# Optimization experiments

Hardware: AMD Instinct MI355X
Metric: run time of the kernel (lower is better)

The kernel has to match this reference:

```python
import jax, jax.numpy as jnp
import numpy as np

N_SPK, N_UTT, D = 512, 64, 1024
EPS = 1e-6  # matches tf.math.l2_normalize default epsilon guard


def _l2norm(x, axis=-1):
    return x / jnp.sqrt(jnp.maximum(jnp.sum(x * x, axis=axis, keepdims=True), EPS))


def setup_inputs() -> dict:
    key = jax.random.key(0)
    k1, _ = jax.random.split(key)
    inputs = jax.random.normal(k1, (N_SPK, N_UTT, D), dtype=jnp.float32)
    w = jnp.asarray(10.0, dtype=jnp.float32)
    b = jnp.asarray(-5.0, dtype=jnp.float32)
    return {"inputs": inputs, "w": w, "b": b}


def reference(inputs, w, b):
    N, M, _ = inputs.shape
    # speaker centroids: mean over utterances -> [N, D]
    centroids = jnp.mean(inputs, axis=1)
    # utterance (exclusion) centroids: mean of the other M-1 utterances -> [N, M, D]
    ut_centroids = (jnp.sum(inputs, axis=1, keepdims=True) - inputs) / (M - 1)

    e = _l2norm(inputs)          # [N, M, D]
    c = _l2norm(centroids)       # [N, D]
    uc = _l2norm(ut_centroids)   # [N, M, D]

    # cosine sim of every utterance vs every speaker centroid -> [N, M, K]
    cos_all = jnp.einsum('nmd,kd->nmk', e, c)
    # same-speaker entries use the self-exclusion centroid
    cos_self = jnp.sum(e * uc, axis=-1)  # [N, M]
    eye = jnp.eye(N, dtype=inputs.dtype)[:, None, :]  # [N, 1, N]
    cos_sim = cos_all * (1.0 - eye) + cos_self[:, :, None] * eye

    sim = w * cos_sim + b  # [N, M, N]
    # softmax contrastive loss: -S_{j,i,j} + logsumexp_k S_{j,i,k}, summed
    lse = jax.nn.logsumexp(sim, axis=-1)            # [N, M]
    pos = jnp.einsum('nmn->nm', sim)                # diagonal along speaker axes
    loss = jnp.sum(lse - pos)
    return loss
```

## Files before the change

kernel.cpp:

```cpp
#include <hip/hip_runtime.h>
#include <stdint.h>

#define N_SPK 512
#define N_UTT 64
#define DIM   1024
#define NROWS (N_SPK * N_UTT)
#define EPS   1e-6f

#define BM  128
#define BN  128
#define BKB 128
#define KITERS (DIM / BKB)

typedef __attribute__((ext_vector_type(8))) int   int8v;
typedef __attribute__((ext_vector_type(4))) int   int4v;
typedef __attribute__((ext_vector_type(4))) float f32x4;

__global__ __launch_bounds__(256) void prep_full(
    const float* __restrict__ x, uint8_t* __restrict__ xb,
    uint8_t* __restrict__ cmat, float* __restrict__ xxg, float* __restrict__ ssqg)
{
    const int n    = blockIdx.x;
    const int tid  = threadIdx.x;
    const int lane = tid & 63;
    const int w    = tid >> 6;

    const float* xn  = x  + (size_t)n * N_UTT * DIM;
    uint8_t*     xbn = xb + (size_t)n * N_UTT * DIM;

    float Sp[16];
    #pragma unroll
    for (int j = 0; j < 16; ++j) Sp[j] = 0.f;

    for (int rnd = 0; rnd < 4; ++rnd) {
        const int m0 = w * 16 + rnd * 4;

        float4 v[16];
        #pragma unroll
        for (int i = 0; i < 4; ++i)
            #pragma unroll
            for (int j = 0; j < 4; ++j)
                v[i * 4 + j] = *(const float4*)(xn + (size_t)(m0 + i) * DIM + j * 256 + lane * 4);

        float xx[4] = {0.f, 0.f, 0.f, 0.f};
        #pragma unroll
        for (int i = 0; i < 4; ++i) {
            #pragma unroll
            for (int j = 0; j < 4; ++j) {
                const float4 q = v[i * 4 + j];
                xx[i] += q.x * q.x + q.y * q.y + q.z * q.z + q.w * q.w;
                Sp[j * 4 + 0] += q.x; Sp[j * 4 + 1] += q.y;
                Sp[j * 4 + 2] += q.z; Sp[j * 4 + 3] += q.w;
                uint32_t u = (uint32_t)__builtin_amdgcn_cvt_pk_fp8_f32(q.x, q.y, 0, false);
                u = (uint32_t)__builtin_amdgcn_cvt_pk_fp8_f32(q.z, q.w, (int)u, true);
                *(uint32_t*)(xbn + (size_t)(m0 + i) * DIM + j * 256 + lane * 4) = u;
            }
        }

        #pragma unroll
        for (int i = 0; i < 4; ++i) {
            float t = xx[i];
            #pragma unroll
            for (int off = 1; off < 64; off <<= 1) t += __shfl_xor(t, off);
            if (lane == 0) xxg[n * N_UTT + m0 + i] = t;
        }
    }

    __shared__ float Sh[4][DIM];
    #pragma unroll
    for (int j = 0; j < 4; ++j)
        *(float4*)&Sh[w][j * 256 + lane * 4] =
            make_float4(Sp[j * 4], Sp[j * 4 + 1], Sp[j * 4 + 2], Sp[j * 4 + 3]);
    __syncthreads();

    const int d0 = tid * 4;
    float4 S = *(const float4*)&Sh[0][d0];
    {
        const float4 b1 = *(const float4*)&Sh[1][d0];
        const float4 b2 = *(const float4*)&Sh[2][d0];
        const float4 b3 = *(const float4*)&Sh[3][d0];
        S.x += b1.x + b2.x + b3.x; S.y += b1.y + b2.y + b3.y;
        S.z += b1.z + b2.z + b3.z; S.w += b1.w + b2.w + b3.w;
    }

    float css = S.x * S.x + S.y * S.y + S.z * S.z + S.w * S.w;
    #pragma unroll
    for (int off = 1; off < 64; off <<= 1) css += __shfl_xor(css, off);
    __shared__ float red[4];
    if ((tid & 63) == 0) red[tid >> 6] = css;
    __syncthreads();
    const float ssq = red[0] + red[1] + red[2] + red[3];

    const float scale = rsqrtf(fmaxf(ssq * (1.0f / 4096.f), EPS)) * (16.0f / 64.f);
    uint32_t u = (uint32_t)__builtin_amdgcn_cvt_pk_fp8_f32(S.x * scale, S.y * scale, 0, false);
    u = (uint32_t)__builtin_amdgcn_cvt_pk_fp8_f32(S.z * scale, S.w * scale, (int)u, true);
    *(uint32_t*)(cmat + (size_t)n * DIM + d0) = u;
    if (tid == 0) ssqg[n] = ssq;
}

__global__ __launch_bounds__(256) void gemm_lse_kernel(
    const uint8_t* __restrict__ xb, const uint8_t* __restrict__ cmat,
    const float* __restrict__ xxg, const float* __restrict__ ssqg,
    const float* __restrict__ wp, const float* __restrict__ bp,
    float* __restrict__ sumexp4, float* __restrict__ pos)
{
    __shared__ __align__(16) uint8_t Asm[BM * BKB];
    __shared__ __align__(16) uint8_t Bsm[BN * BKB];
    __shared__ float SeLDS[BM];

    const int tid   = threadIdx.x;
    const int lane  = tid & 63;
    const int wid   = tid >> 6;
    const int waveM = wid >> 1;
    const int waveN = wid & 1;

    const int bid = blockIdx.x;
    const int rt  = (bid & 7) | ((bid >> 5) << 3);
    const int ct  = (bid >> 3) & 3;

    const int rowBase = rt * BM;
    const int colBase = ct * BN;

    const uint8_t* gA[4];
    const uint8_t* gB[4];
    #pragma unroll
    for (int i = 0; i < 4; ++i) {
        const int s    = i * 256 + tid;
        const int srow = s >> 3;
        const int h    = (s & 7) ^ (srow & 7);
        gA[i] = xb   + (size_t)(rowBase + srow) * DIM + h * 16;
        gB[i] = cmat + (size_t)(colBase + srow) * DIM + h * 16;
    }

    f32x4 acc[4][4];
    #pragma unroll
    for (int i = 0; i < 4; ++i)
        #pragma unroll
        for (int j = 0; j < 4; ++j)
            acc[i][j] = (f32x4){0.f, 0.f, 0.f, 0.f};

    const int cL  = lane & 15;
    const int q   = lane >> 4;
    const int fs0 = (2 * q) ^ (cL & 7);
    const int fs1 = fs0 ^ 1;

    for (int kt = 0; kt < KITERS; ++kt) {
        __syncthreads();
        const int ko = kt * BKB;
        #pragma unroll
        for (int i = 0; i < 4; ++i) {
            __builtin_amdgcn_global_load_lds(
                (const __attribute__((address_space(1))) void*)(gA[i] + ko),
                (__attribute__((address_space(3))) void*)(&Asm[(i * 256 + wid * 64) * 16]),
                16, 0, 0);
            __builtin_amdgcn_global_load_lds(
                (const __attribute__((address_space(1))) void*)(gB[i] + ko),
                (__attribute__((address_space(3))) void*)(&Bsm[(i * 256 + wid * 64) * 16]),
                16, 0, 0);
        }
        __syncthreads();

        int8v b[4];
        #pragma unroll
        for (int bj = 0; bj < 4; ++bj) {
            const int row = waveN * 64 + bj * 16 + cL;
            const int4v lo = *(const int4v*)&Bsm[row * BKB + fs0 * 16];
            const int4v hi = *(const int4v*)&Bsm[row * BKB + fs1 * 16];
            b[bj] = __builtin_shufflevector(lo, hi, 0, 1, 2, 3, 4, 5, 6, 7);
        }

        #pragma unroll
        for (int bi = 0; bi < 4; ++bi) {
            const int row = waveM * 64 + bi * 16 + cL;
            const int4v lo = *(const int4v*)&Asm[row * BKB + fs0 * 16];
            const int4v hi = *(const int4v*)&Asm[row * BKB + fs1 * 16];
            const int8v a = __builtin_shufflevector(lo, hi, 0, 1, 2, 3, 4, 5, 6, 7);
            #pragma unroll
            for (int bj = 0; bj < 4; ++bj)
                acc[bi][bj] = __builtin_amdgcn_mfma_scale_f32_16x16x128_f8f6f4(
                    a, b[bj], acc[bi][bj],
                    0, 0,
                    0, 0x7f7f7f7f,
                    0, 0x7f7f7f7f);
        }
    }

    const float wv = wp[0] * 0.0625f;
    const float bv = bp[0];
    float srow[16];
    #pragma unroll
    for (int bi = 0; bi < 4; ++bi) {
        #pragma unroll
        for (int r = 0; r < 4; ++r) {
            const int R     = rowBase + waveM * 64 + bi * 16 + q * 4 + r;
            const float xxv = xxg[R];
            const float rn  = rsqrtf(fmaxf(xxv, EPS));
            const int nrow  = R >> 6;
            float s = 0.f;
            #pragma unroll
            for (int bj = 0; bj < 4; ++bj) {
                const int col = colBase + waveN * 64 + bj * 16 + cL;
                const float dot = acc[bi][bj][r];
                float sim;
                if (col == nrow) {
                    const float ssqv = ssqg[nrow];
                    const float xs   = dot * sqrtf(ssqv) * 0.0625f;
                    const float d2   = ssqv - 2.f * xs + xxv;
                    const float cs   = ((xs - xxv) * (1.f / 63.f)) * rn *
                                       rsqrtf(fmaxf(d2 * (1.f / 3969.f), EPS));
                    sim = wp[0] * cs + bv;
                    pos[R] = sim;
                } else {
                    sim = wv * dot * rn + bv;
                }
                s += __expf(sim);
            }
            #pragma unroll
            for (int off = 1; off < 16; off <<= 1) s += __shfl_xor(s, off);
            srow[bi * 4 + r] = s;
        }
    }

    if (waveN == 1 && cL == 0) {
        #pragma unroll
        for (int bi = 0; bi < 4; ++bi)
            #pragma unroll
            for (int r = 0; r < 4; ++r)
                SeLDS[waveM * 64 + bi * 16 + q * 4 + r] = srow[bi * 4 + r];
    }
    __syncthreads();
    if (waveN == 0 && cL == 0) {
        #pragma unroll
        for (int bi = 0; bi < 4; ++bi)
            #pragma unroll
            for (int r = 0; r < 4; ++r) {
                const int lr = waveM * 64 + bi * 16 + q * 4 + r;
                sumexp4[(size_t)ct * NROWS + rowBase + lr] = srow[bi * 4 + r] + SeLDS[lr];
            }
    }
}

__global__ __launch_bounds__(1024) void finalize_kernel(
    const float* __restrict__ pos, const float* __restrict__ se4,
    float* __restrict__ out)
{
    const int tid = threadIdx.x;
    float acc = 0.f;
    for (int r = tid; r < NROWS; r += 1024) {
        const float s = se4[r] + se4[NROWS + r] + se4[2 * NROWS + r] + se4[3 * NROWS + r];
        acc += __logf(s) - pos[r];
    }
    #pragma unroll
    for (int off = 1; off < 64; off <<= 1) acc += __shfl_xor(acc, off);
    __shared__ float red[16];
    if ((tid & 63) == 0) red[tid >> 6] = acc;
    __syncthreads();
    if (tid == 0) {
        float t = 0.f;
        #pragma unroll
        for (int i = 0; i < 16; ++i) t += red[i];
        out[0] = t;
    }
}

extern "C" void kernel_launch(void* const* d_in, const int* in_sizes, int n_in,
                              void* d_out, int out_size, void* d_ws, size_t ws_size,
                              hipStream_t stream)
{
    const float* x  = (const float*)d_in[0];
    const float* wp = (const float*)d_in[1];
    const float* bp = (const float*)d_in[2];
    float* out = (float*)d_out;

    char* ws = (char*)d_ws;
    size_t off = 0;
    uint8_t*  xb      = (uint8_t*)(ws + off); off += (size_t)NROWS * DIM;
    uint8_t*  cmat    = (uint8_t*)(ws + off); off += (size_t)N_SPK * DIM;
    float*    xxg     = (float*)(ws + off);   off += (size_t)NROWS * 4;
    float*    pos     = (float*)(ws + off);   off += (size_t)NROWS * 4;
    float*    sumexp4 = (float*)(ws + off);   off += (size_t)4 * NROWS * 4;
    float*    ssqg    = (float*)(ws + off);   off += (size_t)N_SPK * 4;

    prep_full<<<N_SPK, 256, 0, stream>>>(x, xb, cmat, xxg, ssqg);
    gemm_lse_kernel<<<(NROWS / BM) * (N_SPK / BN), 256, 0, stream>>>(
        xb, cmat, xxg, ssqg, wp, bp, sumexp4, pos);
    finalize_kernel<<<1, 1024, 0, stream>>>(pos, sumexp4, out);
}
```

Measured before the change: 278.8 us.

## Process two column tiles per GEMM block, deepen prep loads, parallelize finalize

The GEMM grid is halved so each block loops over two consecutive column tiles. The A tile is reloaded for each tile, so this only changes scheduling and block count, with fewer blocks over the 256 CUs. The prep kernel now issues eight rows of loads per round instead of four, giving more memory-level parallelism at higher register cost. The finalize reduction is spread over 64 blocks that atomically add into an output zeroed by the prep kernel, which removes the serial single-block tail but makes the float summation order nondeterministic.

```diff
diff --git a/kernel.cpp b/kernel.cpp
--- a/kernel.cpp
+++ b/kernel.cpp
@@ -18,13 +18,16 @@
 
 __global__ __launch_bounds__(256) void prep_full(
     const float* __restrict__ x, uint8_t* __restrict__ xb,
-    uint8_t* __restrict__ cmat, float* __restrict__ xxg, float* __restrict__ ssqg)
+    uint8_t* __restrict__ cmat, float* __restrict__ xxg, float* __restrict__ ssqg,
+    float* __restrict__ out)
 {
     const int n    = blockIdx.x;
     const int tid  = threadIdx.x;
     const int lane = tid & 63;
     const int w    = tid >> 6;
 
+    if (n == 0 && tid == 0) out[0] = 0.f;
+
     const float* xn  = x  + (size_t)n * N_UTT * DIM;
     uint8_t*     xbn = xb + (size_t)n * N_UTT * DIM;
 
@@ -32,19 +35,22 @@
     #pragma unroll
     for (int j = 0; j < 16; ++j) Sp[j] = 0.f;
 
-    for (int rnd = 0; rnd < 4; ++rnd) {
-        const int m0 = w * 16 + rnd * 4;
-
-        float4 v[16];
-        #pragma unroll
-        for (int i = 0; i < 4; ++i)
+    for (int rnd = 0; rnd < 2; ++rnd) {
+        const int m0 = w * 16 + rnd * 8;
+
+        float4 v[32];
+        #pragma unroll
+        for (int i = 0; i < 8; ++i)
             #pragma unroll
             for (int j = 0; j < 4; ++j)
                 v[i * 4 + j] = *(const float4*)(xn + (size_t)(m0 + i) * DIM + j * 256 + lane * 4);
 
-        float xx[4] = {0.f, 0.f, 0.f, 0.f};
-        #pragma unroll
-        for (int i = 0; i < 4; ++i) {
+        float xx[8];
+        #pragma unroll
+        for (int i = 0; i < 8; ++i) xx[i] = 0.f;
+
+        #pragma unroll
+        for (int i = 0; i < 8; ++i) {
             #pragma unroll
             for (int j = 0; j < 4; ++j) {
                 const float4 q = v[i * 4 + j];
@@ -58,7 +64,7 @@
         }
 
         #pragma unroll
-        for (int i = 0; i < 4; ++i) {
+        for (int i = 0; i < 8; ++i) {
             float t = xx[i];
             #pragma unroll
             for (int off = 1; off < 64; off <<= 1) t += __shfl_xor(t, off);
@@ -114,153 +120,148 @@
     const int waveM = wid >> 1;
     const int waveN = wid & 1;
 
-    const int bid = blockIdx.x;
-    const int rt  = (bid & 7) | ((bid >> 5) << 3);
-    const int ct  = (bid >> 3) & 3;
-
+    const int p     = blockIdx.x;
+    const int rt    = (p & 7) | ((p >> 4) << 3);
+    const int cpair = (p >> 3) & 1;
     const int rowBase = rt * BM;
-    const int colBase = ct * BN;
-
-    const uint8_t* gA[4];
-    const uint8_t* gB[4];
-    #pragma unroll
-    for (int i = 0; i < 4; ++i) {
-        const int s    = i * 256 + tid;
-        const int srow = s >> 3;
-        const int h    = (s & 7) ^ (srow & 7);
-        gA[i] = xb   + (size_t)(rowBase + srow) * DIM + h * 16;
-        gB[i] = cmat + (size_t)(colBase + srow) * DIM + h * 16;
-    }
-
-    f32x4 acc[4][4];
-    #pragma unroll
-    for (int i = 0; i < 4; ++i)
-        #pragma unroll
-        for (int j = 0; j < 4; ++j)
-            acc[i][j] = (f32x4){0.f, 0.f, 0.f, 0.f};
+
+    const int srow0 = tid >> 3;
+    const int h     = (tid & 7) ^ (srow0 & 7);
+    const uint8_t* gA0 = xb + (size_t)(rowBase + srow0) * DIM + h * 16;
 
     const int cL  = lane & 15;
     const int q   = lane >> 4;
     const int fs0 = (2 * q) ^ (cL & 7);
     const int fs1 = fs0 ^ 1;
 
-    for (int kt = 0; kt < KITERS; ++kt) {
+    const float wv0 = wp[0];
+    const float wv  = wv0 * 0.0625f;
+    const float bv  = bp[0];
+
+    for (int t = 0; t < 2; ++t) {
+        const int ct      = cpair * 2 + t;
+        const int colBase = ct * BN;
+        const uint8_t* gB0 = cmat + (size_t)(colBase + srow0) * DIM + h * 16;
+
+        f32x4 acc[4][4];
+        #pragma unroll
+        for (int i = 0; i < 4; ++i)
+            #pragma unroll
+            for (int j = 0; j < 4; ++j)
+                acc[i][j] = (f32x4){0.f, 0.f, 0.f, 0.f};
+
+        for (int kt = 0; kt < KITERS; ++kt) {
+            __syncthreads();
+            const int ko = kt * BKB;
+            #pragma unroll
+            for (int i = 0; i < 4; ++i) {
+                __builtin_amdgcn_global_load_lds(
+                    (const __attribute__((address_space(1))) void*)(gA0 + (size_t)i * 32 * DIM + ko),
+                    (__attribute__((address_space(3))) void*)(&Asm[(i * 256 + wid * 64) * 16]),
+                    16, 0, 0);
+                __builtin_amdgcn_global_load_lds(
+                    (const __attribute__((address_space(1))) void*)(gB0 + (size_t)i * 32 * DIM + ko),
+                    (__attribute__((address_space(3))) void*)(&Bsm[(i * 256 + wid * 64) * 16]),
+                    16, 0, 0);
+            }
+            __syncthreads();
+
+            int8v b[4];
+            #pragma unroll
+            for (int bj = 0; bj < 4; ++bj) {
+                const int row = waveN * 64 + bj * 16 + cL;
+                const int4v lo = *(const int4v*)&Bsm[row * BKB + fs0 * 16];
+                const int4v hi = *(const int4v*)&Bsm[row * BKB + fs1 * 16];
+                b[bj] = __builtin_shufflevector(lo, hi, 0, 1, 2, 3, 4, 5, 6, 7);
+            }
+
+            #pragma unroll
+            for (int bi = 0; bi < 4; ++bi) {
+                const int row = waveM * 64 + bi * 16 + cL;
+                const int4v lo = *(const int4v*)&Asm[row * BKB + fs0 * 16];
+                const int4v hi = *(const int4v*)&Asm[row * BKB + fs1 * 16];
+                const int8v a = __builtin_shufflevector(lo, hi, 0, 1, 2, 3, 4, 5, 6, 7);
+                #pragma unroll
+                for (int bj = 0; bj < 4; ++bj)
+                    acc[bi][bj] = __builtin_amdgcn_mfma_scale_f32_16x16x128_f8f6f4(
+                        a, b[bj], acc[bi][bj],
+                        0, 0,
+                        0, 0x7f7f7f7f,
+                        0, 0x7f7f7f7f);
+            }
+        }
+
+        float srow[16];
+        #pragma unroll
+        for (int bi = 0; bi < 4; ++bi) {
+            #pragma unroll
+            for (int r = 0; r < 4; ++r) {
+                const int R     = rowBase + waveM * 64 + bi * 16 + q * 4 + r;
+                const float xxv = xxg[R];
+                const float rn  = rsqrtf(fmaxf(xxv, EPS));
+                const int nrow  = R >> 6;
+                float s = 0.f;
+                #pragma unroll
+                for (int bj = 0; bj < 4; ++bj) {
+                    const int col = colBase + waveN * 64 + bj * 16 + cL;
+                    const float dot = acc[bi][bj][r];
+                    float sim;
+                    if (col == nrow) {
+                        const float ssqv = ssqg[nrow];
+                        const float xs   = dot * sqrtf(ssqv) * 0.0625f;
+                        const float d2   = ssqv - 2.f * xs + xxv;
+                        const float cs   = ((xs - xxv) * (1.f / 63.f)) * rn *
+                                           rsqrtf(fmaxf(d2 * (1.f / 3969.f), EPS));
+                        sim = wv0 * cs + bv;
+                        pos[R] = sim;
+                    } else {
+                        sim = wv * dot * rn + bv;
+                    }
+                    s += __expf(sim);
+                }
+                #pragma unroll
+                for (int off = 1; off < 16; off <<= 1) s += __shfl_xor(s, off);
+                srow[bi * 4 + r] = s;
+            }
+        }
+
+        if (waveN == 1 && cL == 0) {
+            #pragma unroll
+            for (int bi = 0; bi < 4; ++bi)
+                #pragma unroll
+                for (int r = 0; r < 4; ++r)
+                    SeLDS[waveM * 64 + bi * 16 + q * 4 + r] = srow[bi * 4 + r];
+        }
         __syncthreads();
-        const int ko = kt * BKB;
-        #pragma unroll
-        for (int i = 0; i < 4; ++i) {
-            __builtin_amdgcn_global_load_lds(
-                (const __attribute__((address_space(1))) void*)(gA[i] + ko),
-                (__attribute__((address_space(3))) void*)(&Asm[(i * 256 + wid * 64) * 16]),
-                16, 0, 0);
-            __builtin_amdgcn_global_load_lds(
-                (const __attribute__((address_space(1))) void*)(gB[i] + ko),
-                (__attribute__((address_space(3))) void*)(&Bsm[(i * 256 + wid * 64) * 16]),
-                16, 0, 0);
-        }
-        __syncthreads();
-
-        int8v b[4];
-        #pragma unroll
-        for (int bj = 0; bj < 4; ++bj) {
-            const int row = waveN * 64 + bj * 16 + cL;
-            const int4v lo = *(const int4v*)&Bsm[row * BKB + fs0 * 16];
-            const int4v hi = *(const int4v*)&Bsm[row * BKB + fs1 * 16];
-            b[bj] = __builtin_shufflevector(lo, hi, 0, 1, 2, 3, 4, 5, 6, 7);
-        }
-
-        #pragma unroll
-        for (int bi = 0; bi < 4; ++bi) {
-            const int row = waveM * 64 + bi * 16 + cL;
-            const int4v lo = *(const int4v*)&Asm[row * BKB + fs0 * 16];
-            const int4v hi = *(const int4v*)&Asm[row * BKB + fs1 * 16];
-            const int8v a = __builtin_shufflevector(lo, hi, 0, 1, 2, 3, 4, 5, 6, 7);
-            #pragma unroll
-            for (int bj = 0; bj < 4; ++bj)
-                acc[bi][bj] = __builtin_amdgcn_mfma_scale_f32_16x16x128_f8f6f4(
-                    a, b[bj], acc[bi][bj],
-                    0, 0,
-                    0, 0x7f7f7f7f,
-                    0, 0x7f7f7f7f);
-        }
-    }
-
-    const float wv = wp[0] * 0.0625f;
-    const float bv = bp[0];
-    float srow[16];
-    #pragma unroll
-    for (int bi = 0; bi < 4; ++bi) {
-        #pragma unroll
-        for (int r = 0; r < 4; ++r) {
-            const int R     = rowBase + waveM * 64 + bi * 16 + q * 4 + r;
-            const float xxv = xxg[R];
-            const float rn  = rsqrtf(fmaxf(xxv, EPS));
-            const int nrow  = R >> 6;
-            float s = 0.f;
-            #pragma unroll
-            for (int bj = 0; bj < 4; ++bj) {
-                const int col = colBase + waveN * 64 + bj * 16 + cL;
-                const float dot = acc[bi][bj][r];
-                float sim;
-                if (col == nrow) {
-                    const float ssqv = ssqg[nrow];
-                    const float xs   = dot * sqrtf(ssqv) * 0.0625f;
-                    const float d2   = ssqv - 2.f * xs + xxv;
-                    const float cs   = ((xs - xxv) * (1.f / 63.f)) * rn *
-                                       rsqrtf(fmaxf(d2 * (1.f / 3969.f), EPS));
-                    sim = wp[0] * cs + bv;
-                    pos[R] = sim;
-                } else {
-                    sim = wv * dot * rn + bv;
+        if (waveN == 0 && cL == 0) {
+            #pragma unroll
+            for (int bi = 0; bi < 4; ++bi)
+                #pragma unroll
+                for (int r = 0; r < 4; ++r) {
+                    const int lr = waveM * 64 + bi * 16 + q * 4 + r;
+                    sumexp4[(size_t)ct * NROWS + rowBase + lr] = srow[bi * 4 + r] + SeLDS[lr];
                 }
-                s += __expf(sim);
-            }
-            #pragma unroll
-            for (int off = 1; off < 16; off <<= 1) s += __shfl_xor(s, off);
-            srow[bi * 4 + r] = s;
-        }
-    }
-
-    if (waveN == 1 && cL == 0) {
-        #pragma unroll
-        for (int bi = 0; bi < 4; ++bi)
-            #pragma unroll
-            for (int r = 0; r < 4; ++r)
-                SeLDS[waveM * 64 + bi * 16 + q * 4 + r] = srow[bi * 4 + r];
-    }
-    __syncthreads();
-    if (waveN == 0 && cL == 0) {
-        #pragma unroll
-        for (int bi = 0; bi < 4; ++bi)
-            #pragma unroll
-            for (int r = 0; r < 4; ++r) {
-                const int lr = waveM * 64 + bi * 16 + q * 4 + r;
-                sumexp4[(size_t)ct * NROWS + rowBase + lr] = srow[bi * 4 + r] + SeLDS[lr];
-            }
-    }
-}
-
-__global__ __launch_bounds__(1024) void finalize_kernel(
+        }
+    }
+}
+
+__global__ __launch_bounds__(256) void finalize_kernel(
     const float* __restrict__ pos, const float* __restrict__ se4,
     float* __restrict__ out)
 {
-    const int tid = threadIdx.x;
+    const int tid = blockIdx.x * 256 + threadIdx.x;
     float acc = 0.f;
-    for (int r = tid; r < NROWS; r += 1024) {
+    for (int r = tid; r < NROWS; r += 64 * 256) {
         const float s = se4[r] + se4[NROWS + r] + se4[2 * NROWS + r] + se4[3 * NROWS + r];
         acc += __logf(s) - pos[r];
     }
     #pragma unroll
     for (int off = 1; off < 64; off <<= 1) acc += __shfl_xor(acc, off);
-    __shared__ float red[16];
-    if ((tid & 63) == 0) red[tid >> 6] = acc;
+    __shared__ float red[4];
+    if ((threadIdx.x & 63) == 0) red[threadIdx.x >> 6] = acc;
     __syncthreads();
-    if (tid == 0) {
-        float t = 0.f;
-        #pragma unroll
-        for (int i = 0; i < 16; ++i) t += red[i];
-        out[0] = t;
-    }
+    if (threadIdx.x == 0)
+        atomicAdd(out, red[0] + red[1] + red[2] + red[3]);
 }
 
 extern "C" void kernel_launch(void* const* d_in, const int* in_sizes, int n_in,
@@ -281,8 +282,8 @@
     float*    sumexp4 = (float*)(ws + off);   off += (size_t)4 * NROWS * 4;
     float*    ssqg    = (float*)(ws + off);   off += (size_t)N_SPK * 4;
 
-    prep_full<<<N_SPK, 256, 0, stream>>>(x, xb, cmat, xxg, ssqg);
-    gemm_lse_kernel<<<(NROWS / BM) * (N_SPK / BN), 256, 0, stream>>>(
+    prep_full<<<N_SPK, 256, 0, stream>>>(x, xb, cmat, xxg, ssqg, out);
+    gemm_lse_kernel<<<(NROWS / BM) * 2, 256, 0, stream>>>(
         xb, cmat, xxg, ssqg, wp, bp, sumexp4, pos);
-    finalize_kernel<<<1, 1024, 0, stream>>>(pos, sumexp4, out);
-}
+    finalize_kernel<<<64, 256, 0, stream>>>(pos, sumexp4, out);
+}
```

After: 327.9 us. 17.6% more time.
